# Optimization experiments

Hardware: AMD Instinct MI355X
Metric: run time of the kernel (lower is better)

## Reference

```python
import jax, jax.numpy as jnp
import numpy as np

LAYER_NUM = 2
NUM_CLS = 128
HIDDEN = 256
NUM_NODES = 1024


def setup_inputs() -> dict:
    key = jax.random.key(0)
    ks = jax.random.split(key, 12)
    s = 0.05
    return {
        "x": jax.random.normal(ks[0], (NUM_NODES, HIDDEN), jnp.float32),
        "knowledge": jax.random.uniform(ks[1], (NUM_CLS, NUM_CLS), jnp.float32) / NUM_CLS,
        "w3w": jax.random.normal(ks[2], (HIDDEN, 2 * HIDDEN), jnp.float32) * s,
        "b3w": jax.random.normal(ks[3], (HIDDEN,), jnp.float32) * s,
        "u3": jax.random.normal(ks[4], (HIDDEN, HIDDEN), jnp.float32) * s,
        "bu3": jax.random.normal(ks[5], (HIDDEN,), jnp.float32) * s,
        "w4w": jax.random.normal(ks[6], (HIDDEN, 2 * HIDDEN), jnp.float32) * s,
        "b4w": jax.random.normal(ks[7], (HIDDEN,), jnp.float32) * s,
        "w5w": jax.random.normal(ks[8], (HIDDEN, 2 * HIDDEN), jnp.float32) * s,
        "b5w": jax.random.normal(ks[9], (HIDDEN,), jnp.float32) * s,
        "u5": jax.random.normal(ks[10], (HIDDEN, HIDDEN), jnp.float32) * s,
        "bu5": jax.random.normal(ks[11], (HIDDEN,), jnp.float32) * s,
    }


def reference(x, knowledge, w3w, b3w, u3, bu3, w4w, b4w, w5w, b5w, u5, bu5):
    N, H = x.shape
    C = knowledge.shape[0]
    # hidden[n, c, :] = x[n, :]  (repeat per class)
    hidden = jnp.broadcast_to(x[:, None, :], (N, C, H))
    for _ in range(LAYER_NUM):
        hs = hidden.sum(0)                      # [C, H]
        diff = hs[None, :, :] - hidden          # [N, C, H]
        # knowledge.T @ diff_n  and  knowledge @ diff_n, vectorized over nodes
        left = jnp.einsum('kc,nkh->nch', knowledge, diff)
        right = jnp.einsum('ck,nkh->nch', knowledge, diff)
        av = jnp.concatenate([left, right], axis=-1).reshape(N * C, 2 * H)
        h = hidden.reshape(N * C, H)
        uh3 = h @ u3.T + bu3                    # shared: rv uses fc_eq3_u (source quirk)
        zv = jax.nn.sigmoid(av @ w3w.T + b3w + uh3)
        rv = jax.nn.sigmoid(av @ w4w.T + b4w + uh3)
        hv = jnp.tanh(av @ w5w.T + b5w + (rv * h) @ u5.T + bu5)
        h = (1.0 - zv) * h + zv * hv
        hidden = h.reshape(N, C, H)
    return hidden
```

## Files before the change

kernel.cpp:

```cpp
#include <hip/hip_runtime.h>
#include <cstdint>
#include <cstddef>


#define NODES 1024
#define NCLS  128
#define HID   256

using frag  = __attribute__((ext_vector_type(8))) short;
using frag4 = __attribute__((ext_vector_type(4))) short;
using f32x4 = __attribute__((ext_vector_type(4))) float;

__device__ __forceinline__ float bf2f(unsigned short h){
  unsigned int u = ((unsigned int)h) << 16;
  float f; __builtin_memcpy(&f, &u, 4); return f;
}
__device__ __forceinline__ unsigned short f2bf(float f){
  unsigned int u; __builtin_memcpy(&u, &f, 4);
  u = (u + 0x7fffu + ((u >> 16) & 1u)) >> 16;
  return (unsigned short)u;
}
__device__ __forceinline__ float sigm(float x){ return 1.0f/(1.0f + __expf(-x)); }
__device__ __forceinline__ float tanh_fast(float x){ return 1.0f - 2.0f/(__expf(2.0f*x) + 1.0f); }

#define GLOBAL_AS(p) ((const __attribute__((address_space(1))) void*)(p))
#define LDS_AS(p)    ((__attribute__((address_space(3))) void*)(p))
#define MFMA16 __builtin_amdgcn_mfma_f32_16x16x32_bf16

template<int OUT_BF16>
__global__ __launch_bounds__(256) void gemm_bf16(
    const unsigned short* __restrict__ A0, int ldA0, int K0,
    const unsigned short* __restrict__ A1, int ldA1,
    const unsigned short* __restrict__ BT, int ldB, long bStride,
    void* __restrict__ Cptr, int ldC,
    int Ntiles, int Ktot, unsigned int aMask, int Mtiles)
{
  __shared__ unsigned short As[4096];
  __shared__ unsigned short Bs[4096];
  const int t   = threadIdx.x;
  const int bid = blockIdx.x;
  const int xcd = bid & 7, slot = bid >> 3;
  const int mtPerX = (Mtiles >= 8) ? (Mtiles >> 3) : 1;
  const int mt = xcd * mtPerX + slot / Ntiles;
  const int nt = slot % Ntiles;
  const int lane = t & 63, w = t >> 6;
  const int wm = w >> 1, wn = w & 1;
  const int r = lane & 15, q = lane >> 4;
  const int m0 = mt * 128, n0 = nt * 128;
  const unsigned short* Bbase = BT + (size_t)mt * (size_t)bStride;

  f32x4 acc[4][4] = {};

  for (int kb = 0; kb < Ktot; kb += 32) {
#pragma unroll
    for (int i = 0; i < 2; ++i) {
      int u  = i * 256 + t;
      int mi = u >> 2;
      int kc = (u & 3) * 8;
      int k  = kb + kc;
      const unsigned short* ga;
      if (k < K0) ga = A0 + (size_t)((unsigned int)(m0 + mi) & aMask) * (size_t)ldA0 + k;
      else        ga = A1 + (size_t)(m0 + mi) * (size_t)ldA1 + (k - K0);
      __builtin_amdgcn_global_load_lds(GLOBAL_AS(ga), LDS_AS(&As[u * 8]), 16, 0, 0);
      const unsigned short* gb = Bbase + (size_t)(n0 + mi) * (size_t)ldB + k;
      __builtin_amdgcn_global_load_lds(GLOBAL_AS(gb), LDS_AS(&Bs[u * 8]), 16, 0, 0);
    }
    __syncthreads();

    frag af[4], bf_[4];
#pragma unroll
    for (int x = 0; x < 4; ++x) {
      af[x]  = *(const frag*)&As[(wm * 64 + x * 16 + r) * 32 + q * 8];
      bf_[x] = *(const frag*)&Bs[(wn * 64 + x * 16 + r) * 32 + q * 8];
    }
#pragma unroll
    for (int x = 0; x < 4; ++x)
#pragma unroll
      for (int y = 0; y < 4; ++y)
        acc[x][y] = MFMA16(af[x], bf_[y], acc[x][y], 0, 0, 0);
    __syncthreads();
  }

#pragma unroll
  for (int x = 0; x < 4; ++x) {
#pragma unroll
    for (int y = 0; y < 4; ++y) {
      int col = n0 + wn * 64 + y * 16 + r;
#pragma unroll
      for (int g = 0; g < 4; ++g) {
        long row = m0 + wm * 64 + x * 16 + q * 4 + g;
        if (OUT_BF16) ((unsigned short*)Cptr)[row * (long)ldC + col] = f2bf(acc[x][y][g]);
        else          ((float*)Cptr)[row * (long)ldC + col] = acc[x][y][g];
      }
    }
  }
}

__global__ __launch_bounds__(512, 2) void gemm_pre(
    const unsigned short* __restrict__ AVH, const unsigned short* __restrict__ H1,
    const unsigned short* __restrict__ WB, const float* __restrict__ SG,
    unsigned short* __restrict__ PRE)
{
  __shared__ __align__(16) unsigned short SM[65536];
  const int t   = threadIdx.x;
  const int bid = blockIdx.x;
  const int xcd = bid & 7, slot = bid >> 3;
  const int mt = xcd * 64 + slot / 3;
  const int ct = slot % 3;
  const int lane = t & 63, w = t >> 6;
  const int wm = w >> 2, wn = w & 3;
  const int r = lane & 15, q = lane >> 4;
  const int m0 = mt * 256;
  const unsigned short* Wrow = WB + (size_t)(ct * 256) * 768;
  const int nkt = (ct < 2) ? 12 : 8;

  unsigned short* const Ab0 = SM;
  unsigned short* const Ab1 = SM + 16384;
  unsigned short* const Bb0 = SM + 32768;
  unsigned short* const Bb1 = SM + 49152;

  f32x4 acc[8][4] = {};

  const int smi = t >> 3, sc = t & 7;

  auto ISSUE_A = [&](unsigned short* dst, int kt, int rbase) {
    int row = rbase + smi;
    int gc = sc ^ (row & 7);
    const unsigned short* ga;
    if (kt < 8) ga = AVH + (size_t)(m0 + row) * 512 + kt * 64 + gc * 8;
    else        ga = H1  + (size_t)(m0 + row) * 256 + (kt - 8) * 64 + gc * 8;
    __builtin_amdgcn_global_load_lds(GLOBAL_AS(ga), LDS_AS(&dst[row * 64 + sc * 8]), 16, 0, 0);
  };
  auto ISSUE_B = [&](unsigned short* dst, int kt, int rbase) {
    int row = rbase + smi;
    int gc = sc ^ (row & 7);
    __builtin_amdgcn_global_load_lds(GLOBAL_AS(Wrow + (size_t)row * 768 + kt * 64 + gc * 8),
                                     LDS_AS(&dst[row * 64 + sc * 8]), 16, 0, 0);
  };

  ISSUE_B(Bb0, 0, 0); ISSUE_B(Bb0, 0, 64); ISSUE_B(Bb0, 0, 128); ISSUE_B(Bb0, 0, 192);
  ISSUE_A(Ab0, 0, 0); ISSUE_A(Ab0, 0, 128); ISSUE_A(Ab0, 0, 64); ISSUE_A(Ab0, 0, 192);
  asm volatile("s_waitcnt vmcnt(2)" ::: "memory");
  __builtin_amdgcn_s_barrier();

#define PRE_PHASE(XG0, ISSUES, TAIL)                                         \
    {                                                                        \
      int ra0 = wm * 128 + (XG0) * 16 + r, ra1 = ra0 + 16;                   \
      frag a00 = *(const frag*)&A[ra0 * 64 + ((q ^ (ra0 & 7)) * 8)];         \
      frag a01 = *(const frag*)&A[ra0 * 64 + (((4 + q) ^ (ra0 & 7)) * 8)];   \
      frag a10 = *(const frag*)&A[ra1 * 64 + ((q ^ (ra1 & 7)) * 8)];         \
      frag a11 = *(const frag*)&A[ra1 * 64 + (((4 + q) ^ (ra1 & 7)) * 8)];   \
      ISSUES;                                                                \
      __builtin_amdgcn_s_setprio(1);                                         \
      _Pragma("unroll")                                                      \
      for (int y = 0; y < 4; ++y) {                                          \
        acc[(XG0)][y]     = MFMA16(a00, bf[y][0], acc[(XG0)][y], 0, 0, 0);   \
        acc[(XG0)][y]     = MFMA16(a01, bf[y][1], acc[(XG0)][y], 0, 0, 0);   \
        acc[(XG0)+1][y]   = MFMA16(a10, bf[y][0], acc[(XG0)+1][y], 0, 0, 0); \
        acc[(XG0)+1][y]   = MFMA16(a11, bf[y][1], acc[(XG0)+1][y], 0, 0, 0); \
      }                                                                      \
      __builtin_amdgcn_s_setprio(0);                                         \
      TAIL;                                                                  \
      asm volatile("" ::: "memory");                                         \
      __builtin_amdgcn_s_barrier();                                          \
    }

  for (int kt = 0; kt < nkt; ++kt) {
    unsigned short* A  = (kt & 1) ? Ab1 : Ab0;
    unsigned short* B  = (kt & 1) ? Bb1 : Bb0;
    unsigned short* An = (kt & 1) ? Ab0 : Ab1;
    unsigned short* Bn = (kt & 1) ? Bb0 : Bb1;
    const bool more = (kt + 1 < nkt);

    frag bf[4][2];
#pragma unroll
    for (int y = 0; y < 4; ++y) {
      int rb = wn * 64 + y * 16 + r;
      bf[y][0] = *(const frag*)&B[rb * 64 + ((q ^ (rb & 7)) * 8)];
      bf[y][1] = *(const frag*)&B[rb * 64 + (((4 + q) ^ (rb & 7)) * 8)];
    }

    PRE_PHASE(0,
      { if (more) { ISSUE_B(Bn, kt + 1, 0); ISSUE_B(Bn, kt + 1, 64); } },
      { })
    PRE_PHASE(2,
      { if (more) { ISSUE_B(Bn, kt + 1, 128); ISSUE_B(Bn, kt + 1, 192); } },
      { if (more) asm volatile("s_waitcnt vmcnt(4)" ::: "memory");
        else      asm volatile("s_waitcnt vmcnt(0)" ::: "memory"); })
    PRE_PHASE(4,
      { if (more) { ISSUE_A(An, kt + 1, 0); ISSUE_A(An, kt + 1, 128); } },
      { })
    PRE_PHASE(6,
      { if (more) { ISSUE_A(An, kt + 1, 64); ISSUE_A(An, kt + 1, 192); } },
      { if (more) asm volatile("s_waitcnt vmcnt(2)" ::: "memory"); })
  }
#undef PRE_PHASE

  unsigned short* L = SM;
#pragma unroll
  for (int xg = 0; xg < 8; ++xg) {
#pragma unroll
    for (int y = 0; y < 4; ++y) {
      int j = wn * 64 + y * 16 + r;
      int jc = j >> 3, jl = j & 7;
#pragma unroll
      for (int g = 0; g < 4; ++g) {
        int c = wm * 128 + xg * 16 + q * 4 + g;
        L[c * 256 + ((jc ^ (c & 31)) * 8) + jl] = f2bf(acc[xg][y][g]);
      }
    }
  }
  __syncthreads();
  if (ct == 1) {
#pragma unroll
    for (int rr = 0; rr < 16; ++rr) {
      int unit = rr * 512 + t;
      int row = unit >> 5, ch = unit & 31;
      size_t grow = (size_t)(m0 + row);
      frag v  = *(const frag*)&L[row * 256 + ((ch ^ (row & 31)) * 8)];
      frag hh = *(const frag*)(H1 + grow * 256 + ch * 8);
      const float* sgr = SG + (size_t)(row & 127) * 768 + 256 + ch * 8;
      f32x4 s0 = *(const f32x4*)(sgr);
      f32x4 s1 = *(const f32x4*)(sgr + 4);
      frag o;
#pragma unroll
      for (int e = 0; e < 8; ++e) {
        float sv = (e < 4) ? s0[e] : s1[e - 4];
        float rv = sigm(sv + bf2f((unsigned short)v[e]));
        o[e] = (short)f2bf(rv * bf2f((unsigned short)hh[e]));
      }
      *(frag*)&PRE[grow * 768 + 256 + ch * 8] = o;
    }
  } else {
#pragma unroll
    for (int rr = 0; rr < 16; ++rr) {
      int unit = rr * 512 + t;
      int row = unit >> 5, ch = unit & 31;
      frag v = *(const frag*)&L[row * 256 + ((ch ^ (row & 31)) * 8)];
      *(frag*)&PRE[(size_t)(m0 + row) * 768 + ct * 256 + ch * 8] = v;
    }
  }
}

__global__ __launch_bounds__(256, 2) void gemm_l1(
    const float* __restrict__ XW, const float* __restrict__ SW,
    const float* __restrict__ x,
    const float* __restrict__ b3, const float* __restrict__ b4,
    const float* __restrict__ b5, const float* __restrict__ bu3,
    const float* __restrict__ bu5,
    const float* __restrict__ colsum, const float* __restrict__ rowsum,
    const unsigned short* __restrict__ u5b,
    const unsigned short* __restrict__ KTbN, const unsigned short* __restrict__ KbN,
    unsigned short* __restrict__ H1, unsigned short* __restrict__ AVH)
{
  __shared__ unsigned short SM[17408];
  unsigned short* L  = SM;
  __shared__ float tP1[256], tP2[256], tP3[256], tX[256];
  __shared__ float tZ1[256], tZ2[256], tZ3[256];
  __shared__ float tV1[256], tV2[256], tV3[256];
  __shared__ float tCS[128], tRS[128];

  const int t = threadIdx.x, bid = blockIdx.x;
  const int xcd = bid & 7, slot = bid >> 3;
  const int n  = xcd * 128 + (slot >> 1);
  const int nt = slot & 1;
  const int lane = t & 63, w = t >> 6, wm = w >> 1, wn = w & 1;
  const int r = lane & 15, q = lane >> 4;
  const int n0 = nt * 128;
  const float* xw = XW + (size_t)n * 1792;

  {
    int i = t;
    float xwi0 = xw[i], xwi1 = xw[256 + i], xwi2 = xw[512 + i], xwi3 = xw[768 + i];
    float xwi4 = xw[1024 + i], xwi5 = xw[1280 + i], xwu = xw[1536 + i];
    tP1[i] = SW[512 + i] - xwi2;
    tP2[i] = SW[768 + i] - xwi3;
    tP3[i] = xwu + b4[i] + bu3[i];
    tX[i]  = x[(size_t)n * HID + i];
    tZ1[i] = SW[i] - xwi0;
    tZ2[i] = SW[256 + i] - xwi1;
    tZ3[i] = xwu + b3[i] + bu3[i];
    tV1[i] = SW[1024 + i] - xwi4;
    tV2[i] = SW[1280 + i] - xwi5;
    tV3[i] = b5[i] + bu5[i];
    if (t < 128) { tCS[t] = colsum[t]; tRS[t] = rowsum[t]; }
  }
  __syncthreads();

  auto PREP_A = [&](unsigned short* Asb, int kb) {
#pragma unroll
    for (int i = 0; i < 2; ++i) {
      int u  = i * 256 + t;
      int mi = u >> 2;
      int c  = u & 3;
      int k  = kb + c * 8;
      int gc = c ^ ((mi >> 1) & 3);
      float cs = tCS[mi], rs = tRS[mi];
      frag a;
#pragma unroll
      for (int e = 0; e < 8; ++e) {
        int i2 = k + e;
        float pre = cs * tP1[i2] + rs * tP2[i2] + tP3[i2];
        a[e] = (short)f2bf(sigm(pre) * tX[i2]);
      }
      *(frag*)&Asb[mi * 32 + (gc * 8)] = a;
    }
  };
  auto STAGE_B = [&](unsigned short* Bsb, int kb) {
#pragma unroll
    for (int i = 0; i < 2; ++i) {
      int u  = i * 256 + t;
      int mi = u >> 2;
      int c  = u & 3;
      int gc = c ^ ((mi >> 1) & 3);
      __builtin_amdgcn_global_load_lds(GLOBAL_AS(u5b + (size_t)(n0 + mi) * 256 + kb + gc * 8),
                                       LDS_AS(&Bsb[u * 8]), 16, 0, 0);
    }
  };

  PREP_A(SM, 0);
  STAGE_B(SM + 8192, 0);
  __syncthreads();

  f32x4 acc[4][4] = {};

  for (int kb = 0; kb < 256; kb += 32) {
    const int cur = (kb >> 5) & 1;
    const unsigned short* Asb = SM + cur * 4096;
    const unsigned short* Bsb = SM + 8192 + cur * 4096;

    frag af[4], bf_[4];
#pragma unroll
    for (int xx = 0; xx < 4; ++xx) {
      int ra = wm * 64 + xx * 16 + r;
      int rb = wn * 64 + xx * 16 + r;
      af[xx]  = *(const frag*)&Asb[ra * 32 + ((q ^ ((ra >> 1) & 3)) * 8)];
      bf_[xx] = *(const frag*)&Bsb[rb * 32 + ((q ^ ((rb >> 1) & 3)) * 8)];
    }

    if (kb < 224) {
      STAGE_B(SM + 8192 + (cur ^ 1) * 4096, kb + 32);
      PREP_A(SM + (cur ^ 1) * 4096, kb + 32);
    }

#pragma unroll
    for (int xx = 0; xx < 4; ++xx)
#pragma unroll
      for (int y = 0; y < 4; ++y)
        acc[xx][y] = MFMA16(af[xx], bf_[y], acc[xx][y], 0, 0, 0);
    __syncthreads();
  }

#pragma unroll
  for (int xx = 0; xx < 4; ++xx) {
#pragma unroll
    for (int y = 0; y < 4; ++y) {
      int j = wn * 64 + y * 16 + r;
      int i = n0 + j;
      frag4 pack;
#pragma unroll
      for (int g = 0; g < 4; ++g) {
        int c = wm * 64 + xx * 16 + q * 4 + g;
        float cs = tCS[c], rs = tRS[c];
        float z  = sigm(cs * tZ1[i] + rs * tZ2[i] + tZ3[i]);
        float p5 = cs * tV1[i] + rs * tV2[i] + tV3[i] + acc[xx][y][g];
        float h1 = (1.0f - z) * tX[i] + z * tanh_fast(p5);
        unsigned short hb = f2bf(h1);
        pack[g] = (short)hb;
        H1[(size_t)(n * 128 + c) * HID + i] = hb;
      }
      *(frag4*)&L[j * 136 + (wm * 64 + xx * 16 + q * 4)] = pack;
    }
  }
  __syncthreads();

#pragma unroll 1
  for (int s = 0; s < 2; ++s) {
    const unsigned short* Ks = s ? KbN : KTbN;
#pragma unroll
    for (int xx = 0; xx < 4; ++xx)
#pragma unroll
      for (int y = 0; y < 4; ++y)
        acc[xx][y] = (f32x4){0.0f, 0.0f, 0.0f, 0.0f};
#pragma unroll
    for (int kb = 0; kb < 4; ++kb) {
      frag af[4], bf_[4];
#pragma unroll
      for (int xx = 0; xx < 4; ++xx) {
        int cp = wm * 64 + xx * 16 + r;
        af[xx] = *(const frag*)(Ks + (size_t)cp * 128 + kb * 32 + q * 8);
        int j = wn * 64 + xx * 16 + r;
        bf_[xx] = *(const frag*)&L[j * 136 + kb * 32 + q * 8];
      }
#pragma unroll
      for (int xx = 0; xx < 4; ++xx)
#pragma unroll
        for (int y = 0; y < 4; ++y)
          acc[xx][y] = MFMA16(af[xx], bf_[y], acc[xx][y], 0, 0, 0);
    }
#pragma unroll
    for (int xx = 0; xx < 4; ++xx)
#pragma unroll
      for (int y = 0; y < 4; ++y) {
        int col = s * 256 + n0 + wn * 64 + y * 16 + r;
#pragma unroll
        for (int g = 0; g < 4; ++g) {
          int cp = wm * 64 + xx * 16 + q * 4 + g;
          AVH[(size_t)(n * 128 + cp) * 512 + col] = f2bf(acc[xx][y][g]);
        }
      }
  }
}

__global__ __launch_bounds__(256, 3) void gemm_l2(
    const unsigned short* __restrict__ PRE, const float* __restrict__ SG,
    const unsigned short* __restrict__ H1, const unsigned short* __restrict__ u5b,
    float* __restrict__ out)
{
  __shared__ __align__(16) unsigned short SM[16384];
  unsigned short* const As = SM;
  unsigned short* const Bs = SM + 4096;
  float* L = (float*)SM;

  const int t = threadIdx.x, bid = blockIdx.x;
  const int xcd = bid & 7, slot = bid >> 3;
  const int mt = xcd * 128 + (slot >> 1);
  const int nt = slot & 1;
  const int lane = t & 63, w = t >> 6, wm = w >> 1, wn = w & 1;
  const int r = lane & 15, q = lane >> 4;
  const int m0 = mt * 128, n0 = nt * 128;

  f32x4 acc[4][4] = {};

  for (int kb = 0; kb < 256; kb += 32) {
#pragma unroll
    for (int i = 0; i < 2; ++i) {
      int u  = i * 256 + t;
      int mi = u >> 2;
      int gc = (u & 3) ^ ((mi >> 1) & 3);
      __builtin_amdgcn_global_load_lds(GLOBAL_AS(PRE + (size_t)(m0 + mi) * 768 + 256 + kb + gc * 8),
                                       LDS_AS(&As[u * 8]), 16, 0, 0);
      __builtin_amdgcn_global_load_lds(GLOBAL_AS(u5b + (size_t)(n0 + mi) * 256 + kb + gc * 8),
                                       LDS_AS(&Bs[u * 8]), 16, 0, 0);
    }
    __syncthreads();

    frag af[4], bf_[4];
#pragma unroll
    for (int xx = 0; xx < 4; ++xx) {
      int ra = wm * 64 + xx * 16 + r;
      int rb = wn * 64 + xx * 16 + r;
      af[xx]  = *(const frag*)&As[ra * 32 + ((q ^ ((ra >> 1) & 3)) * 8)];
      bf_[xx] = *(const frag*)&Bs[rb * 32 + ((q ^ ((rb >> 1) & 3)) * 8)];
    }
#pragma unroll
    for (int xx = 0; xx < 4; ++xx)
#pragma unroll
      for (int y = 0; y < 4; ++y)
        acc[xx][y] = MFMA16(af[xx], bf_[y], acc[xx][y], 0, 0, 0);
    __syncthreads();
  }

  const int lr_r = t >> 2;
  const int cb   = t & 3;
#pragma unroll 1
  for (int p = 0; p < 2; ++p) {
    if (p) __syncthreads();
    if (wm == p) {
#pragma unroll
      for (int xx = 0; xx < 4; ++xx)
#pragma unroll
        for (int y = 0; y < 4; ++y) {
          int j = wn * 64 + y * 16 + r;
#pragma unroll
          for (int g = 0; g < 4; ++g) {
            int lr = xx * 16 + q * 4 + g;
            L[lr * 128 + (j ^ ((lr & 7) << 2))] = acc[xx][y][g];
          }
        }
    }
    __syncthreads();
    long grow = m0 + p * 64 + lr_r;
    int cc = (int)(grow & 127);
    const unsigned short* prow = PRE + (size_t)grow * 768;
    const unsigned short* hrow = H1 + (size_t)grow * 256;
    const float* sgr = SG + (size_t)cc * 768;
    const int off = (lr_r & 7) << 2;
#pragma unroll
    for (int gi = 0; gi < 4; ++gi) {
      int j0 = cb * 8 + gi * 32;
      int i0 = n0 + j0;
      f32x4 a0 = *(const f32x4*)&L[lr_r * 128 + (j0 ^ off)];
      f32x4 a1 = *(const f32x4*)&L[lr_r * 128 + ((j0 + 4) ^ off)];
      frag pz = *(const frag*)(prow + i0);
      frag pp = *(const frag*)(prow + 512 + i0);
      frag hh = *(const frag*)(hrow + i0);
      f32x4 sz0 = *(const f32x4*)(sgr + i0);
      f32x4 sz1 = *(const f32x4*)(sgr + i0 + 4);
      f32x4 sp0 = *(const f32x4*)(sgr + 512 + i0);
      f32x4 sp1 = *(const f32x4*)(sgr + 512 + i0 + 4);
      f32x4 o0, o1;
#pragma unroll
      for (int e = 0; e < 8; ++e) {
        float sz = (e < 4) ? sz0[e] : sz1[e - 4];
        float sp = (e < 4) ? sp0[e] : sp1[e - 4];
        float av = (e < 4) ? a0[e] : a1[e - 4];
        float z  = sigm(sz + bf2f((unsigned short)pz[e]));
        float pv = sp + bf2f((unsigned short)pp[e]) + av;
        float h  = bf2f((unsigned short)hh[e]);
        float o  = (1.0f - z) * h + z * tanh_fast(pv);
        if (e < 4) o0[e] = o; else o1[e - 4] = o;
      }
      *(f32x4*)&out[(size_t)grow * 256 + i0] = o0;
      *(f32x4*)&out[(size_t)grow * 256 + i0 + 4] = o1;
    }
  }
}

__global__ __launch_bounds__(256) void prep_cast(
    const float* __restrict__ x, const float* __restrict__ Kn,
    const float* __restrict__ w3, const float* __restrict__ u3,
    const float* __restrict__ w4, const float* __restrict__ w5,
    const float* __restrict__ u5,
    unsigned short* __restrict__ xb, unsigned short* __restrict__ WB,
    unsigned short* __restrict__ WB2, unsigned short* __restrict__ u5b,
    unsigned short* __restrict__ KbN, unsigned short* __restrict__ KTbN)
{
  int idx = blockIdx.x * 256 + threadIdx.x;
  if (idx < 262144) { xb[idx] = f2bf(x[idx]); return; }
  idx -= 262144;
  if (idx < 589824) {
    int col = idx / 768, j = idx % 768;
    int g = col >> 8, i = col & 255;
    float v;
    if (j < 512) { const float* wg = (g == 0) ? w3 : (g == 1) ? w4 : w5; v = wg[(size_t)i * 512 + j]; }
    else v = (g < 2) ? u3[(size_t)i * 256 + (j - 512)] : 0.0f;
    WB[(size_t)col * 768 + j] = f2bf(v);
    return;
  }
  idx -= 589824;
  if (idx < 458752) {
    int col = idx / 256, h = idx % 256;
    int b = col >> 8, i = col & 255;
    float v = (b < 6) ? ((b < 2 ? w3 : (b < 4 ? w4 : w5))[(size_t)i * 512 + (b & 1) * 256 + h])
                      : u3[(size_t)i * 256 + h];
    WB2[(size_t)col * 256 + h] = f2bf(v);
    return;
  }
  idx -= 458752;
  if (idx < 65536) { u5b[idx] = f2bf(u5[idx]); return; }
  idx -= 65536;
  if (idx < 16384) { int c = idx >> 7, k = idx & 127; KbN[idx]  = f2bf(-Kn[c * 128 + k]); return; }
  idx -= 16384;
  { int c = idx >> 7, k = idx & 127; KTbN[idx] = f2bf(-Kn[k * 128 + c]); }
}

__global__ __launch_bounds__(256) void prep_reduce(
    const float* __restrict__ x, const float* __restrict__ Kn,
    float* __restrict__ S, float* __restrict__ colsum, float* __restrict__ rowsum)
{
  int b = blockIdx.x, t = threadIdx.x;
  if (b < 8) {
    float s = 0.f;
    for (int n = 0; n < 128; ++n) s += x[(size_t)(b * 128 + n) * HID + t];
    atomicAdd(&S[t], s);
  } else if (b == 8) {
    if (t < NCLS) { float s = 0.f; for (int k = 0; k < NCLS; ++k) s += Kn[k * NCLS + t]; colsum[t] = s; }
  } else {
    if (t < NCLS) { float s = 0.f; for (int k = 0; k < NCLS; ++k) s += Kn[t * NCLS + k]; rowsum[t] = s; }
  }
}

__global__ __launch_bounds__(256) void prep_sw(
    const float* __restrict__ S, const float* __restrict__ w3,
    const float* __restrict__ w4, const float* __restrict__ w5, float* __restrict__ SW)
{
  int col = blockIdx.x * 256 + threadIdx.x;
  int b = col >> 8, i = col & 255;
  const float* w = (b < 2) ? w3 : (b < 4) ? w4 : w5;
  const float* row = w + (size_t)i * 512 + (b & 1) * 256;
  float s = 0.f;
  for (int h = 0; h < HID; ++h) s += S[h] * row[h];
  SW[col] = s;
}

__global__ __launch_bounds__(256) void reduce_hs(
    const unsigned short* __restrict__ H1, float* __restrict__ hs)
{
  int bid = blockIdx.x;
  int c = bid >> 5, nch = bid & 31;
  int i = threadIdx.x;
  const unsigned short* p = H1 + (size_t)nch * 32 * NCLS * HID + (size_t)c * HID + i;
  float s = 0.f;
  for (int n = 0; n < 32; ++n) s += bf2f(p[(size_t)n * NCLS * HID]);
  atomicAdd(&hs[c * HID + i], s);
}

__global__ __launch_bounds__(256) void p2a(
    const float* __restrict__ hs, const float* __restrict__ w3,
    const float* __restrict__ w4, const float* __restrict__ w5, float* __restrict__ hsW)
{
  __shared__ float hrow[HID];
  int k = blockIdx.x & 127, b = blockIdx.x >> 7;
  int t = threadIdx.x;
  hrow[t] = hs[k * HID + t];
  __syncthreads();
  const float* w = (b < 2) ? w3 : (b < 4) ? w4 : w5;
  const float* row = w + (size_t)t * 512 + (b & 1) * 256;
  float s = 0.f;
  for (int h = 0; h < HID; ++h) s += hrow[h] * row[h];
  hsW[(size_t)k * 1536 + b * 256 + t] = s;
}

__global__ __launch_bounds__(256) void p2b(
    const float* __restrict__ hsW, const float* __restrict__ Kn,
    const float* __restrict__ b3, const float* __restrict__ b4, const float* __restrict__ b5,
    const float* __restrict__ bu3, const float* __restrict__ bu5, float* __restrict__ SG)
{
  __shared__ float kc[NCLS], kr[NCLS];
  int c = blockIdx.x, t = threadIdx.x;
  if (t < NCLS) { kc[t] = Kn[t * NCLS + c]; kr[t] = Kn[c * NCLS + t]; }
  __syncthreads();
  for (int g = 0; g < 3; ++g) {
    int i = t;
    const float* L = hsW + (size_t)(2 * g) * 256 + i;
    const float* R = hsW + (size_t)(2 * g + 1) * 256 + i;
    float s = 0.f;
    for (int k = 0; k < NCLS; ++k) s += kc[k] * L[(size_t)k * 1536] + kr[k] * R[(size_t)k * 1536];
    const float* bg = (g == 0) ? b3 : (g == 1) ? b4 : b5;
    s += bg[i] + ((g < 2) ? bu3[i] : bu5[i]);
    SG[(size_t)c * 768 + g * 256 + i] = s;
  }
}

extern "C" void kernel_launch(void* const* d_in, const int* in_sizes, int n_in,
                              void* d_out, int out_size, void* d_ws, size_t ws_size,
                              hipStream_t stream) {
  (void)in_sizes; (void)n_in; (void)out_size; (void)ws_size;
  const float* x   = (const float*)d_in[0];
  const float* Kn  = (const float*)d_in[1];
  const float* w3  = (const float*)d_in[2];
  const float* b3  = (const float*)d_in[3];
  const float* u3  = (const float*)d_in[4];
  const float* bu3 = (const float*)d_in[5];
  const float* w4  = (const float*)d_in[6];
  const float* b4  = (const float*)d_in[7];
  const float* w5  = (const float*)d_in[8];
  const float* b5  = (const float*)d_in[9];
  const float* u5  = (const float*)d_in[10];
  const float* bu5 = (const float*)d_in[11];
  float* out = (float*)d_out;

  char* w = (char*)d_ws;
  unsigned short* AVH = (unsigned short*)(w);
  unsigned short* PRE = (unsigned short*)(w + 134217728);
  unsigned short* H1  = (unsigned short*)(w + 335544320);
  float*          XW  = (float*)(w + 402653184);
  char* misc = w + 409993216;
  float* S      = (float*)(misc);
  float* hs     = (float*)(misc + 1024);
  float* SW     = (float*)(misc + 132096);
  float* colsum = (float*)(misc + 138240);
  float* rowsum = (float*)(misc + 138752);
  float* hsW    = (float*)(misc + 139264);
  float* SG     = (float*)(misc + 925696);
  unsigned short* WB   = (unsigned short*)(misc + 1318912);
  unsigned short* WB2  = (unsigned short*)(misc + 2498560);
  unsigned short* u5b  = (unsigned short*)(misc + 3416064);
  unsigned short* KbN  = (unsigned short*)(misc + 3547136);
  unsigned short* KTbN = (unsigned short*)(misc + 3579904);
  unsigned short* xb   = (unsigned short*)(misc + 3612672);

  hipMemsetAsync(misc, 0, 132096, stream);

  prep_cast<<<5504, 256, 0, stream>>>(x, Kn, w3, u3, w4, w5, u5, xb, WB, WB2, u5b, KbN, KTbN);
  prep_reduce<<<10, 256, 0, stream>>>(x, Kn, S, colsum, rowsum);
  prep_sw<<<6, 256, 0, stream>>>(S, w3, w4, w5, SW);

  gemm_bf16<0><<<8 * 14, 256, 0, stream>>>(xb, 256, 256, xb, 256, WB2, 256, 0L,
                                           (void*)XW, 1792, 14, 256, 0xFFFFFFFFu, 8);
  gemm_l1<<<2048, 256, 0, stream>>>(XW, SW, x, b3, b4, b5, bu3, bu5,
                                    colsum, rowsum, u5b, KTbN, KbN, H1, AVH);

  reduce_hs<<<4096, 256, 0, stream>>>(H1, hs);
  p2a<<<768, 256, 0, stream>>>(hs, w3, w4, w5, hsW);
  p2b<<<128, 256, 0, stream>>>(hsW, Kn, b3, b4, b5, bu3, bu5, SG);

  gemm_pre<<<1536, 512, 0, stream>>>(AVH, H1, WB, SG, PRE);

  gemm_l2<<<2048, 256, 0, stream>>>(PRE, SG, H1, u5b, out);
}
```

Measured before the change: 677.5 us.

## Fuse (r*h)@u5 GEMM into gemm_pre and replace gemm_l2 with elementwise

The ct==1 blocks of gemm_pre now keep the rv*h tile in LDS and immediately multiply it by u5 (B operand read straight from global) with MFMA. The bf16 product is written into the PRE middle slot. gemm_l2 becomes a pure elementwise kernel that reads PRE's three slots. This avoids writing the rv*h intermediate and re-reading it for a separate GEMM. In exchange, a third of gemm_pre blocks do extra serial work, which adds load imbalance, and the u5 result is rounded to bf16 before the tanh.

```diff
diff --git a/kernel.cpp b/kernel.cpp
--- a/kernel.cpp
+++ b/kernel.cpp
@@ -99,6 +99,7 @@
 __global__ __launch_bounds__(512, 2) void gemm_pre(
     const unsigned short* __restrict__ AVH, const unsigned short* __restrict__ H1,
     const unsigned short* __restrict__ WB, const float* __restrict__ SG,
+    const unsigned short* __restrict__ u5b,
     unsigned short* __restrict__ PRE)
 {
   __shared__ __align__(16) unsigned short SM[65536];
@@ -211,13 +212,15 @@
     }
   }
   __syncthreads();
+
   if (ct == 1) {
 #pragma unroll
     for (int rr = 0; rr < 16; ++rr) {
       int unit = rr * 512 + t;
       int row = unit >> 5, ch = unit & 31;
       size_t grow = (size_t)(m0 + row);
-      frag v  = *(const frag*)&L[row * 256 + ((ch ^ (row & 31)) * 8)];
+      int sw = (ch ^ (row & 31)) * 8;
+      frag v  = *(const frag*)&L[row * 256 + sw];
       frag hh = *(const frag*)(H1 + grow * 256 + ch * 8);
       const float* sgr = SG + (size_t)(row & 127) * 768 + 256 + ch * 8;
       f32x4 s0 = *(const f32x4*)(sgr);
@@ -229,7 +232,55 @@
         float rv = sigm(sv + bf2f((unsigned short)v[e]));
         o[e] = (short)f2bf(rv * bf2f((unsigned short)hh[e]));
       }
-      *(frag*)&PRE[grow * 768 + 256 + ch * 8] = o;
+      *(frag*)&L[row * 256 + sw] = o;
+    }
+    __syncthreads();
+
+#pragma unroll
+    for (int xg = 0; xg < 8; ++xg)
+#pragma unroll
+      for (int y = 0; y < 4; ++y)
+        acc[xg][y] = (f32x4){0.0f, 0.0f, 0.0f, 0.0f};
+#pragma unroll 1
+    for (int kb = 0; kb < 8; ++kb) {
+      frag bf2[4];
+#pragma unroll
+      for (int y = 0; y < 4; ++y) {
+        int rb = wn * 64 + y * 16 + r;
+        bf2[y] = *(const frag*)(u5b + (size_t)rb * 256 + kb * 32 + q * 8);
+      }
+#pragma unroll
+      for (int xg = 0; xg < 8; ++xg) {
+        int ra = wm * 128 + xg * 16 + r;
+        int chn = (kb * 4 + q) ^ (ra & 31);
+        frag a = *(const frag*)&L[ra * 256 + chn * 8];
+#pragma unroll
+        for (int y = 0; y < 4; ++y)
+          acc[xg][y] = MFMA16(a, bf2[y], acc[xg][y], 0, 0, 0);
+      }
+    }
+    __syncthreads();
+
+#pragma unroll
+    for (int xg = 0; xg < 8; ++xg) {
+#pragma unroll
+      for (int y = 0; y < 4; ++y) {
+        int j = wn * 64 + y * 16 + r;
+        int jc = j >> 3, jl = j & 7;
+#pragma unroll
+        for (int g = 0; g < 4; ++g) {
+          int c = wm * 128 + xg * 16 + q * 4 + g;
+          L[c * 256 + ((jc ^ (c & 31)) * 8) + jl] = f2bf(acc[xg][y][g]);
+        }
+      }
+    }
+    __syncthreads();
+#pragma unroll
+    for (int rr = 0; rr < 16; ++rr) {
+      int unit = rr * 512 + t;
+      int row = unit >> 5, ch = unit & 31;
+      frag v = *(const frag*)&L[row * 256 + ((ch ^ (row & 31)) * 8)];
+      *(frag*)&PRE[(size_t)(m0 + row) * 768 + 256 + ch * 8] = v;
     }
   } else {
 #pragma unroll
@@ -412,109 +463,38 @@
   }
 }
 
-__global__ __launch_bounds__(256, 3) void gemm_l2(
+__global__ __launch_bounds__(256) void l2_ew(
     const unsigned short* __restrict__ PRE, const float* __restrict__ SG,
-    const unsigned short* __restrict__ H1, const unsigned short* __restrict__ u5b,
-    float* __restrict__ out)
-{
-  __shared__ __align__(16) unsigned short SM[16384];
-  unsigned short* const As = SM;
-  unsigned short* const Bs = SM + 4096;
-  float* L = (float*)SM;
-
-  const int t = threadIdx.x, bid = blockIdx.x;
-  const int xcd = bid & 7, slot = bid >> 3;
-  const int mt = xcd * 128 + (slot >> 1);
-  const int nt = slot & 1;
-  const int lane = t & 63, w = t >> 6, wm = w >> 1, wn = w & 1;
-  const int r = lane & 15, q = lane >> 4;
-  const int m0 = mt * 128, n0 = nt * 128;
-
-  f32x4 acc[4][4] = {};
-
-  for (int kb = 0; kb < 256; kb += 32) {
-#pragma unroll
-    for (int i = 0; i < 2; ++i) {
-      int u  = i * 256 + t;
-      int mi = u >> 2;
-      int gc = (u & 3) ^ ((mi >> 1) & 3);
-      __builtin_amdgcn_global_load_lds(GLOBAL_AS(PRE + (size_t)(m0 + mi) * 768 + 256 + kb + gc * 8),
-                                       LDS_AS(&As[u * 8]), 16, 0, 0);
-      __builtin_amdgcn_global_load_lds(GLOBAL_AS(u5b + (size_t)(n0 + mi) * 256 + kb + gc * 8),
-                                       LDS_AS(&Bs[u * 8]), 16, 0, 0);
-    }
-    __syncthreads();
-
-    frag af[4], bf_[4];
-#pragma unroll
-    for (int xx = 0; xx < 4; ++xx) {
-      int ra = wm * 64 + xx * 16 + r;
-      int rb = wn * 64 + xx * 16 + r;
-      af[xx]  = *(const frag*)&As[ra * 32 + ((q ^ ((ra >> 1) & 3)) * 8)];
-      bf_[xx] = *(const frag*)&Bs[rb * 32 + ((q ^ ((rb >> 1) & 3)) * 8)];
-    }
-#pragma unroll
-    for (int xx = 0; xx < 4; ++xx)
-#pragma unroll
-      for (int y = 0; y < 4; ++y)
-        acc[xx][y] = MFMA16(af[xx], bf_[y], acc[xx][y], 0, 0, 0);
-    __syncthreads();
-  }
-
-  const int lr_r = t >> 2;
-  const int cb   = t & 3;
-#pragma unroll 1
-  for (int p = 0; p < 2; ++p) {
-    if (p) __syncthreads();
-    if (wm == p) {
-#pragma unroll
-      for (int xx = 0; xx < 4; ++xx)
-#pragma unroll
-        for (int y = 0; y < 4; ++y) {
-          int j = wn * 64 + y * 16 + r;
-#pragma unroll
-          for (int g = 0; g < 4; ++g) {
-            int lr = xx * 16 + q * 4 + g;
-            L[lr * 128 + (j ^ ((lr & 7) << 2))] = acc[xx][y][g];
-          }
-        }
-    }
-    __syncthreads();
-    long grow = m0 + p * 64 + lr_r;
-    int cc = (int)(grow & 127);
-    const unsigned short* prow = PRE + (size_t)grow * 768;
-    const unsigned short* hrow = H1 + (size_t)grow * 256;
-    const float* sgr = SG + (size_t)cc * 768;
-    const int off = (lr_r & 7) << 2;
-#pragma unroll
-    for (int gi = 0; gi < 4; ++gi) {
-      int j0 = cb * 8 + gi * 32;
-      int i0 = n0 + j0;
-      f32x4 a0 = *(const f32x4*)&L[lr_r * 128 + (j0 ^ off)];
-      f32x4 a1 = *(const f32x4*)&L[lr_r * 128 + ((j0 + 4) ^ off)];
-      frag pz = *(const frag*)(prow + i0);
-      frag pp = *(const frag*)(prow + 512 + i0);
-      frag hh = *(const frag*)(hrow + i0);
-      f32x4 sz0 = *(const f32x4*)(sgr + i0);
-      f32x4 sz1 = *(const f32x4*)(sgr + i0 + 4);
-      f32x4 sp0 = *(const f32x4*)(sgr + 512 + i0);
-      f32x4 sp1 = *(const f32x4*)(sgr + 512 + i0 + 4);
-      f32x4 o0, o1;
-#pragma unroll
-      for (int e = 0; e < 8; ++e) {
-        float sz = (e < 4) ? sz0[e] : sz1[e - 4];
-        float sp = (e < 4) ? sp0[e] : sp1[e - 4];
-        float av = (e < 4) ? a0[e] : a1[e - 4];
-        float z  = sigm(sz + bf2f((unsigned short)pz[e]));
-        float pv = sp + bf2f((unsigned short)pp[e]) + av;
-        float h  = bf2f((unsigned short)hh[e]);
-        float o  = (1.0f - z) * h + z * tanh_fast(pv);
-        if (e < 4) o0[e] = o; else o1[e - 4] = o;
-      }
-      *(f32x4*)&out[(size_t)grow * 256 + i0] = o0;
-      *(f32x4*)&out[(size_t)grow * 256 + i0 + 4] = o1;
-    }
-  }
+    const unsigned short* __restrict__ H1, float* __restrict__ out)
+{
+  int idx = blockIdx.x * 256 + threadIdx.x;
+  int row = idx >> 5, ch = idx & 31;
+  size_t grow = (size_t)row;
+  int c = row & 127;
+  int i0 = ch * 8;
+  const unsigned short* prow = PRE + grow * 768;
+  frag pz = *(const frag*)(prow + i0);
+  frag pa = *(const frag*)(prow + 256 + i0);
+  frag pp = *(const frag*)(prow + 512 + i0);
+  frag hh = *(const frag*)(H1 + grow * 256 + i0);
+  const float* sgr = SG + (size_t)c * 768;
+  f32x4 sz0 = *(const f32x4*)(sgr + i0);
+  f32x4 sz1 = *(const f32x4*)(sgr + i0 + 4);
+  f32x4 sp0 = *(const f32x4*)(sgr + 512 + i0);
+  f32x4 sp1 = *(const f32x4*)(sgr + 512 + i0 + 4);
+  f32x4 o0, o1;
+#pragma unroll
+  for (int e = 0; e < 8; ++e) {
+    float sz = (e < 4) ? sz0[e] : sz1[e - 4];
+    float sp = (e < 4) ? sp0[e] : sp1[e - 4];
+    float z  = sigm(sz + bf2f((unsigned short)pz[e]));
+    float pv = sp + bf2f((unsigned short)pp[e]) + bf2f((unsigned short)pa[e]);
+    float h  = bf2f((unsigned short)hh[e]);
+    float o  = (1.0f - z) * h + z * tanh_fast(pv);
+    if (e < 4) o0[e] = o; else o1[e - 4] = o;
+  }
+  *(f32x4*)&out[grow * 256 + i0] = o0;
+  *(f32x4*)&out[grow * 256 + i0 + 4] = o1;
 }
 
 __global__ __launch_bounds__(256) void prep_cast(
@@ -686,7 +666,7 @@
   p2a<<<768, 256, 0, stream>>>(hs, w3, w4, w5, hsW);
   p2b<<<128, 256, 0, stream>>>(hsW, Kn, b3, b4, b5, bu3, bu5, SG);
 
-  gemm_pre<<<1536, 512, 0, stream>>>(AVH, H1, WB, SG, PRE);
-
-  gemm_l2<<<2048, 256, 0, stream>>>(PRE, SG, H1, u5b, out);
-}
+  gemm_pre<<<1536, 512, 0, stream>>>(AVH, H1, WB, SG, u5b, PRE);
+
+  l2_ew<<<16384, 256, 0, stream>>>(PRE, SG, H1, out);
+}
```

After: 691.3 us. 2.0% more time.
